# Kernel tuning notes

Hardware: AMD Instinct MI355X
Metric: run time of the kernel (lower is better)

The kernel has to match this reference:

```python
import jax, jax.numpy as jnp
import numpy as np

N = 16384          # replayed items
D_STATE = 2048     # state_dim
D_SEM = 1024       # semantic_dim
S = 4096           # num_semantic_slots
LR = 0.01
DIST_THRESH = 2.0


def setup_inputs() -> dict:
    key = jax.random.key(0)
    k1, k2, k3 = jax.random.split(key, 3)
    replayed_states = jax.random.normal(k1, (N, D_STATE), dtype=jnp.float32)
    replayed_rewards = jax.random.normal(k2, (N,), dtype=jnp.float32)
    # small weight scale so projected content std ~0.05 -> nearest distances
    # straddle the 2.0 threshold and both branches get exercised
    W = jax.random.normal(k3, (D_SEM, D_STATE), dtype=jnp.float32) * (0.05 / np.sqrt(D_STATE))
    b = jnp.zeros((D_SEM,), dtype=jnp.float32)
    semantic_traces = jnp.zeros((S, D_SEM), dtype=jnp.float32)
    trace_strengths = jnp.zeros((S,), dtype=jnp.float32)
    return {
        "replayed_states": replayed_states,
        "replayed_rewards": replayed_rewards,
        "W": W,
        "b": b,
        "semantic_traces": semantic_traces,
        "trace_strengths": trace_strengths,
    }


def _consolidate(content_all, rewards, traces0, strengths0):
    slot_ids = jnp.arange(S, dtype=jnp.int32)

    def step(carry, xs):
        traces, strengths, ptr, num = carry
        content, reward = xs
        reward = jnp.abs(reward)
        valid = jnp.minimum(num, S)
        # euclidean distances to valid slots (invalid -> +inf)
        d = jnp.sqrt(jnp.sum((traces - content[None, :]) ** 2, axis=1))
        d = jnp.where(slot_ids < valid, d, jnp.inf)
        nearest = jnp.argmin(d).astype(jnp.int32)
        nearest_dist = d[nearest]
        do_update = (num > 0) & (nearest_dist < DIST_THRESH)

        # branch A: EMA update of nearest slot
        eff_lr = LR * (1.0 + reward)
        delta = content - traces[nearest]
        traces_u = traces.at[nearest].add(delta * eff_lr)
        strengths_u = strengths.at[nearest].add(1.0)

        # branch B: insert at ring-buffer ptr
        traces_i = traces.at[ptr].set(content)
        strengths_i = strengths.at[ptr].set(1.0)
        ptr_i = (ptr + 1) % S
        num_i = jnp.minimum(num + 1, S)

        traces_n = jnp.where(do_update, traces_u, traces_i)
        strengths_n = jnp.where(do_update, strengths_u, strengths_i)
        ptr_n = jnp.where(do_update, ptr, ptr_i)
        num_n = jnp.where(do_update, num, num_i)
        return (traces_n, strengths_n, ptr_n, num_n), None

    init = (traces0, strengths0, jnp.int32(0), jnp.int32(0))
    (traces, strengths, ptr, num), _ = jax.lax.scan(step, init, (content_all, rewards))
    return traces, strengths, num


def reference(replayed_states, replayed_rewards, W, b, semantic_traces, trace_strengths):
    # projection: nn.Linear -> x @ W.T + b
    content_all = replayed_states @ W.T + b  # (N, D_SEM)
    traces, strengths, num = _consolidate(
        content_all, replayed_rewards, semantic_traces, trace_strengths
    )
    valid_mask = (jnp.arange(S) < jnp.minimum(num, S)).astype(jnp.float32)
    denom = jnp.maximum(valid_mask.sum(), 1.0)
    mean_strength = jnp.where(num > 0, (strengths * valid_mask).sum() / denom, 0.0)
    num_consolidated = jnp.int32(N)  # every item either updates or inserts
    return traces, strengths, num, num_consolidated, mean_strength


if __name__ == "__main__":
    out = reference(**setup_inputs())
    print([getattr(o, "shape", o) for o in out])
```

## Files before the change

### kernel.cpp

```cpp
#include <hip/hip_runtime.h>
#include <cstdint>
#include <cstddef>

#define N_ITEMS 16384
#define D_STATE 2048
#define D_SEM   1024
#define S_SLOTS 4096
#define DTHRESH 2.0f

#define B_ITEMS 256
#define NBLK    (N_ITEMS / B_ITEMS)
#define CHUNK_BLKS 16
#define CHUNK_ITEMS (B_ITEMS * CHUNK_BLKS)

typedef unsigned long long u64;
typedef unsigned int u32;

__global__ __launch_bounds__(256)
void gemm_kernel(const float* __restrict__ A, const float* __restrict__ W,
                 const float* __restrict__ bias, float* __restrict__ C) {
  __shared__ float As[16][68];
  __shared__ float Bs[16][68];
  const int t = threadIdx.x;
  const int ty = t >> 4, tx = t & 15;
  const int i0 = blockIdx.x * 64, j0 = blockIdx.y * 64;
  const int lrow = t >> 2, lcol = (t & 3) << 2;
  float acc[4][4] = {{0.f}};
  const float* ap = A + (size_t)(i0 + lrow) * D_STATE + lcol;
  const float* wp = W + (size_t)(j0 + lrow) * D_STATE + lcol;
  for (int k0 = 0; k0 < D_STATE; k0 += 16) {
    float4 av = *(const float4*)(ap + k0);
    float4 wv = *(const float4*)(wp + k0);
    __syncthreads();
    As[lcol + 0][lrow] = av.x; As[lcol + 1][lrow] = av.y;
    As[lcol + 2][lrow] = av.z; As[lcol + 3][lrow] = av.w;
    Bs[lcol + 0][lrow] = wv.x; Bs[lcol + 1][lrow] = wv.y;
    Bs[lcol + 2][lrow] = wv.z; Bs[lcol + 3][lrow] = wv.w;
    __syncthreads();
#pragma unroll
    for (int kk = 0; kk < 16; kk++) {
      float a[4], b[4];
#pragma unroll
      for (int y = 0; y < 4; y++) a[y] = As[kk][ty * 4 + y];
#pragma unroll
      for (int x = 0; x < 4; x++) b[x] = Bs[kk][tx * 4 + x];
#pragma unroll
      for (int y = 0; y < 4; y++)
#pragma unroll
        for (int x = 0; x < 4; x++) acc[y][x] = fmaf(a[y], b[x], acc[y][x]);
    }
  }
#pragma unroll
  for (int y = 0; y < 4; y++)
#pragma unroll
    for (int x = 0; x < 4; x++) {
      const int col = j0 + tx * 4 + x;
      C[(size_t)(i0 + ty * 4 + y) * D_SEM + col] = acc[y][x] + bias[col];
    }
}

__global__ __launch_bounds__(256)
void gram_kernel(const float* __restrict__ Cc, float* __restrict__ G) {
  const int z = blockIdx.z;
  const float* A = Cc + (size_t)z * B_ITEMS * D_SEM;
  __shared__ float As[16][68];
  __shared__ float Bs[16][68];
  const int t = threadIdx.x;
  const int ty = t >> 4, tx = t & 15;
  const int i0 = blockIdx.x * 64, j0 = blockIdx.y * 64;
  const int lrow = t >> 2, lcol = (t & 3) << 2;
  float acc[4][4] = {{0.f}};
  const float* ap = A + (size_t)(i0 + lrow) * D_SEM + lcol;
  const float* wp = A + (size_t)(j0 + lrow) * D_SEM + lcol;
  for (int k0 = 0; k0 < D_SEM; k0 += 16) {
    float4 av = *(const float4*)(ap + k0);
    float4 wv = *(const float4*)(wp + k0);
    __syncthreads();
    As[lcol + 0][lrow] = av.x; As[lcol + 1][lrow] = av.y;
    As[lcol + 2][lrow] = av.z; As[lcol + 3][lrow] = av.w;
    Bs[lcol + 0][lrow] = wv.x; Bs[lcol + 1][lrow] = wv.y;
    Bs[lcol + 2][lrow] = wv.z; Bs[lcol + 3][lrow] = wv.w;
    __syncthreads();
#pragma unroll
    for (int kk = 0; kk < 16; kk++) {
      float a[4], b[4];
#pragma unroll
      for (int y = 0; y < 4; y++) a[y] = As[kk][ty * 4 + y];
#pragma unroll
      for (int x = 0; x < 4; x++) b[x] = Bs[kk][tx * 4 + x];
#pragma unroll
      for (int y = 0; y < 4; y++)
#pragma unroll
        for (int x = 0; x < 4; x++) acc[y][x] = fmaf(a[y], b[x], acc[y][x]);
    }
  }
  float* Gz = G + (size_t)z * B_ITEMS * B_ITEMS;
#pragma unroll
  for (int y = 0; y < 4; y++)
#pragma unroll
    for (int x = 0; x < 4; x++)
      Gz[(size_t)(i0 + ty * 4 + y) * B_ITEMS + j0 + tx * 4 + x] = acc[y][x];
}

__global__ __launch_bounds__(256)
void pgemm_kernel(const float* __restrict__ A,
                  const float* __restrict__ T,
                  const float* __restrict__ n_g,
                  float* __restrict__ Q,
                  const int* __restrict__ state) {
  const int limit = min(state[0] + B_ITEMS, S_SLOTS);
  const int j0 = blockIdx.y * 64;
  if (j0 >= limit) return;
  __shared__ float As[16][68];
  __shared__ float Bs[16][68];
  const int t = threadIdx.x;
  const int ty = t >> 4, tx = t & 15;
  const int i0 = blockIdx.x * 64;
  const int lrow = t >> 2, lcol = (t & 3) << 2;
  float acc[4][4] = {{0.f}};
  const float* ap = A + (size_t)(i0 + lrow) * D_SEM + lcol;
  const float* wp = T + (size_t)(j0 + lrow) * D_SEM + lcol;
  for (int k0 = 0; k0 < D_SEM; k0 += 16) {
    float4 av = *(const float4*)(ap + k0);
    float4 wv = *(const float4*)(wp + k0);
    __syncthreads();
    As[lcol + 0][lrow] = av.x; As[lcol + 1][lrow] = av.y;
    As[lcol + 2][lrow] = av.z; As[lcol + 3][lrow] = av.w;
    Bs[lcol + 0][lrow] = wv.x; Bs[lcol + 1][lrow] = wv.y;
    Bs[lcol + 2][lrow] = wv.z; Bs[lcol + 3][lrow] = wv.w;
    __syncthreads();
#pragma unroll
    for (int kk = 0; kk < 16; kk++) {
      float a[4], b[4];
#pragma unroll
      for (int y = 0; y < 4; y++) a[y] = As[kk][ty * 4 + y];
#pragma unroll
      for (int x = 0; x < 4; x++) b[x] = Bs[kk][tx * 4 + x];
#pragma unroll
      for (int y = 0; y < 4; y++)
#pragma unroll
        for (int x = 0; x < 4; x++) acc[y][x] = fmaf(a[y], b[x], acc[y][x]);
    }
  }
#pragma unroll
  for (int y = 0; y < 4; y++)
#pragma unroll
    for (int x = 0; x < 4; x++) {
      const int col = j0 + tx * 4 + x;
      Q[(size_t)(i0 + ty * 4 + y) * S_SLOTS + col] = n_g[col] - 2.0f * acc[y][x];
    }
}

__global__ __launch_bounds__(256)
void init_kernel(const float* __restrict__ traces0, float* __restrict__ out,
                 float* __restrict__ n_g, int* __restrict__ state) {
  __shared__ float wsum[4];
  const int s = blockIdx.x, t = threadIdx.x;
  const int lane = t & 63, wave = t >> 6;
  float4 v = *(const float4*)(traces0 + (size_t)s * D_SEM + 4 * t);
  *(float4*)(out + (size_t)s * D_SEM + 4 * t) = v;
  float nn = v.x * v.x + v.y * v.y + v.z * v.z + v.w * v.w;
#pragma unroll
  for (int o = 32; o; o >>= 1) nn += __shfl_down(nn, o, 64);
  if (lane == 0) wsum[wave] = nn;
  __syncthreads();
  if (t == 0) n_g[s] = wsum[0] + wsum[1] + wsum[2] + wsum[3];
  if (s == 0 && t == 0) { state[0] = 0; state[1] = 0; }
}

__global__ __launch_bounds__(512)
void scan_kernel(float* __restrict__ Q, const float* __restrict__ Gb,
                 const float* __restrict__ rewards, const float* __restrict__ n_g,
                 int* __restrict__ state, u64* __restrict__ decs) {
  __shared__ float n_l[S_SLOTS];
  __shared__ float rew[B_ITEMS];
  __shared__ float gdiag[B_ITEMS];
  __shared__ u64 partials[8];
  __shared__ u32 pub_slotupd;
  __shared__ float pub_lr, pub_nold, pub_nnew;
  __shared__ int sh_num[2], sh_ptr[2];
  __shared__ u32 dslot[B_ITEMS];
  __shared__ float dlr[B_ITEMS];

  const int t = threadIdx.x;
  const int lane = t & 63, wave = t >> 6;

  for (int s = t; s < S_SLOTS; s += 512) n_l[s] = n_g[s];
  if (t < B_ITEMS) {
    rew[t] = rewards[t];
    gdiag[t] = Gb[(size_t)t * B_ITEMS + t];
  }
  if (t == 0) { sh_num[0] = state[0]; sh_ptr[0] = state[1]; }
  float4 n0 = *(const float4*)(Q + 8 * t);
  float4 n1 = *(const float4*)(Q + 8 * t + 4);
  __syncthreads();

  int par = 0;
  for (int i = 0; i < B_ITEMS; i++) {
    float4 c0 = n0, c1 = n1;
    if (i + 1 < B_ITEMS) {
      n0 = *(const float4*)(Q + (size_t)(i + 1) * S_SLOTS + 8 * t);
      n1 = *(const float4*)(Q + (size_t)(i + 1) * S_SLOTS + 8 * t + 4);
    }
    const int num = sh_num[par];
    const float gi = gdiag[i];
    const int s0 = 8 * t;
    u64 best = ~0ull;
#define KEYC(comp, idx) { const int ss = s0 + idx; \
    if (ss < num) { const float d2 = fmaxf(comp + gi, 0.f); \
      const u64 key = ((u64)__float_as_uint(d2) << 32) | (u32)ss; \
      if (key < best) best = key; } }
    KEYC(c0.x, 0) KEYC(c0.y, 1) KEYC(c0.z, 2) KEYC(c0.w, 3)
    KEYC(c1.x, 4) KEYC(c1.y, 5) KEYC(c1.z, 6) KEYC(c1.w, 7)
#undef KEYC
#pragma unroll
    for (int o = 32; o; o >>= 1) {
      const u64 v = __shfl_down(best, o, 64);
      if (v < best) best = v;
    }
    if (lane == 0) partials[wave] = best;
    __syncthreads();

    if (t == 0) {
      u64 bk = partials[0];
#pragma unroll
      for (int wv = 1; wv < 8; wv++) if (partials[wv] < bk) bk = partials[wv];
      const float d2b = __uint_as_float((u32)(bk >> 32));
      const int nslot = (int)(u32)bk;
      const int numc = sh_num[par], ptrc = sh_ptr[par];
      const bool upd = (numc > 0) && (sqrtf(d2b) < DTHRESH);
      const float lr = __fmul_rn(0.01f, __fadd_rn(1.0f, fabsf(rew[i])));
      const int slot = upd ? nslot : ptrc;
      const float n_old = n_l[slot];
      float n_new;
      if (upd) {
        const float omr = 1.0f - lr;
        const float pcur = 0.5f * (n_old + gi - d2b);
        n_new = omr * omr * n_old + 2.0f * lr * omr * pcur + lr * lr * gi;
        sh_num[par ^ 1] = numc; sh_ptr[par ^ 1] = ptrc;
      } else {
        n_new = gi;
        sh_num[par ^ 1] = min(numc + 1, S_SLOTS);
        sh_ptr[par ^ 1] = (ptrc + 1) & (S_SLOTS - 1);
      }
      n_l[slot] = n_new;
      dslot[i] = (u32)slot | (upd ? 0x80000000u : 0u);
      dlr[i] = lr;
      pub_slotupd = (u32)slot | (upd ? 0x80000000u : 0u);
      pub_lr = lr; pub_nold = n_old; pub_nnew = n_new;
    }
    __syncthreads();

    const u32 su = pub_slotupd;
    const int slot = (int)(su & 0x7FFFFFFFu);
    const bool upd = (su & 0x80000000u) != 0;
    const float lr = pub_lr, n_old = pub_nold, n_new = pub_nnew;
    const float omr = 1.0f - lr;
    if (i + 1 < B_ITEMS && t == (slot >> 3)) {
      const float gnext = Gb[(size_t)i * B_ITEMS + (i + 1)];
      const int k = slot & 7;
      float q_old = k == 0 ? n0.x : k == 1 ? n0.y : k == 2 ? n0.z : k == 3 ? n0.w
                  : k == 4 ? n1.x : k == 5 ? n1.y : k == 6 ? n1.z : n1.w;
      const float p_old = 0.5f * (n_old - q_old);
      const float p_new = upd ? (omr * p_old + lr * gnext) : gnext;
      const float q_new = n_new - 2.0f * p_new;
      switch (k) {
        case 0: n0.x = q_new; break; case 1: n0.y = q_new; break;
        case 2: n0.z = q_new; break; case 3: n0.w = q_new; break;
        case 4: n1.x = q_new; break; case 5: n1.y = q_new; break;
        case 6: n1.z = q_new; break; default: n1.w = q_new; break;
      }
    }
    if (t > i + 1 && t < B_ITEMS) {
      const float gv = Gb[(size_t)i * B_ITEMS + t];
      float* qp = Q + (size_t)t * S_SLOTS + slot;
      float p_new;
      if (upd) {
        const float p_old = 0.5f * (n_old - *qp);
        p_new = omr * p_old + lr * gv;
      } else {
        p_new = gv;
      }
      *qp = n_new - 2.0f * p_new;
    }
    par ^= 1;
    __syncthreads();
  }

  if (t == 0) { state[0] = sh_num[par]; state[1] = sh_ptr[par]; }
  if (t < B_ITEMS)
    decs[t] = ((u64)__float_as_uint(dlr[t]) << 32) | (u64)dslot[t];
}

__global__ __launch_bounds__(256)
void apply_kernel(const float* __restrict__ content,
                  const u64* __restrict__ decs,
                  float* __restrict__ traces,
                  float* __restrict__ n_g) {
  __shared__ u32 aslot[B_ITEMS];
  __shared__ float alr[B_ITEMS];
  __shared__ float betas[B_ITEMS];
  __shared__ int notowner;
  __shared__ float wsum[4];
  const int t = threadIdx.x, j = blockIdx.x;
  const int lane = t & 63, wave = t >> 6;
  const u64 d = decs[t];
  aslot[t] = (u32)(d & 0xFFFFFFFFull);
  alr[t] = __uint_as_float((u32)(d >> 32));
  if (t == 0) notowner = 0;
  __syncthreads();
  const u32 myslot = aslot[j] & 0x7FFFFFFFu;
  if (t > j && (aslot[t] & 0x7FFFFFFFu) == myslot) notowner = 1;
  __syncthreads();
  if (notowner) return;

  float alpha = 1.f, beta = 0.f;
  for (int k = 0; k < B_ITEMS; k++) {
    const u32 a = aslot[k];
    if ((a & 0x7FFFFFFFu) == myslot) {
      const float lr = alr[k];
      if (a & 0x80000000u) {
        const float om = 1.f - lr;
        alpha *= om; beta *= om;
        if (t == k) beta += lr;
      } else {
        alpha = 0.f; beta = (t == k) ? 1.f : 0.f;
      }
    }
  }
  betas[t] = beta;
  __syncthreads();

  float4 v = *(const float4*)(traces + (size_t)myslot * D_SEM + 4 * t);
  v.x *= alpha; v.y *= alpha; v.z *= alpha; v.w *= alpha;
  for (int k = 0; k < B_ITEMS; k++) {
    if ((aslot[k] & 0x7FFFFFFFu) == myslot) {
      const float bk = betas[k];
      const float4 c = *(const float4*)(content + (size_t)k * D_SEM + 4 * t);
      v.x = fmaf(bk, c.x, v.x); v.y = fmaf(bk, c.y, v.y);
      v.z = fmaf(bk, c.z, v.z); v.w = fmaf(bk, c.w, v.w);
    }
  }
  *(float4*)(traces + (size_t)myslot * D_SEM + 4 * t) = v;
  float nn = v.x * v.x + v.y * v.y + v.z * v.z + v.w * v.w;
#pragma unroll
  for (int o = 32; o; o >>= 1) nn += __shfl_down(nn, o, 64);
  if (lane == 0) wsum[wave] = nn;
  __syncthreads();
  if (t == 0) n_g[myslot] = wsum[0] + wsum[1] + wsum[2] + wsum[3];
}

__global__ __launch_bounds__(256)
void finalize_kernel(const float* __restrict__ strengths0,
                     const u64* __restrict__ decs,
                     const int* __restrict__ state, float* __restrict__ out) {
  __shared__ float str[S_SLOTS];
  __shared__ u32 dbuf[2048];
  __shared__ float wsum[4];
  const int t = threadIdx.x, lane = t & 63, wave = t >> 6;
  for (int s = t; s < S_SLOTS; s += 256) str[s] = strengths0[s];
  __syncthreads();
  for (int c = 0; c < N_ITEMS; c += 2048) {
    for (int k = t; k < 2048; k += 256) dbuf[k] = (u32)(decs[c + k] & 0xFFFFFFFFull);
    __syncthreads();
    if (t == 0) {
      for (int k = 0; k < 2048; k++) {
        const u32 dd = dbuf[k];
        const int slot = (int)(dd & 0x7FFFFFFFu);
        if (dd & 0x80000000u) str[slot] += 1.f; else str[slot] = 1.f;
      }
    }
    __syncthreads();
  }
  const int num = state[0];
  float* outs = out + (size_t)S_SLOTS * D_SEM;
  float lsum = 0.f;
  for (int s = t; s < S_SLOTS; s += 256) {
    const float v = str[s];
    outs[s] = v;
    if (s < num) lsum += v;
  }
#pragma unroll
  for (int o = 32; o; o >>= 1) lsum += __shfl_down(lsum, o, 64);
  if (lane == 0) wsum[wave] = lsum;
  __syncthreads();
  if (t == 0) {
    const float total = wsum[0] + wsum[1] + wsum[2] + wsum[3];
    float denom = (float)num;
    if (denom < 1.f) denom = 1.f;
    outs[S_SLOTS + 0] = (float)num;
    outs[S_SLOTS + 1] = (float)N_ITEMS;
    outs[S_SLOTS + 2] = (num > 0) ? (total / denom) : 0.f;
  }
}

extern "C" void kernel_launch(void* const* d_in, const int* in_sizes, int n_in,
                              void* d_out, int out_size, void* d_ws, size_t ws_size,
                              hipStream_t stream) {
  const float* states  = (const float*)d_in[0];
  const float* rewards = (const float*)d_in[1];
  const float* W       = (const float*)d_in[2];
  const float* bias    = (const float*)d_in[3];
  const float* traces0 = (const float*)d_in[4];
  const float* str0    = (const float*)d_in[5];
  float* out = (float*)d_out;

  char* p = (char*)d_ws;
  float* cbuf = (float*)p;                 p += (size_t)CHUNK_ITEMS * D_SEM * 4;
  float* Q    = (float*)p;                 p += (size_t)B_ITEMS * S_SLOTS * 4;
  float* Gb   = (float*)p;                 p += (size_t)CHUNK_BLKS * B_ITEMS * B_ITEMS * 4;
  float* n_g  = (float*)p;                 p += (size_t)S_SLOTS * 4;
  u64*   decs = (u64*)p;                   p += (size_t)N_ITEMS * 8;
  int*   state = (int*)p;

  init_kernel<<<S_SLOTS, 256, 0, stream>>>(traces0, out, n_g, state);

  for (int c = 0; c < N_ITEMS / CHUNK_ITEMS; c++) {
    gemm_kernel<<<dim3(CHUNK_ITEMS / 64, D_SEM / 64), 256, 0, stream>>>(
        states + (size_t)c * CHUNK_ITEMS * D_STATE, W, bias, cbuf);
    gram_kernel<<<dim3(4, 4, CHUNK_BLKS), 256, 0, stream>>>(cbuf, Gb);
    for (int bb = 0; bb < CHUNK_BLKS; bb++) {
      const int b = c * CHUNK_BLKS + bb;
      const float* cblk = cbuf + (size_t)bb * B_ITEMS * D_SEM;
      const float* Gblk = Gb + (size_t)bb * B_ITEMS * B_ITEMS;
      pgemm_kernel<<<dim3(4, S_SLOTS / 64), 256, 0, stream>>>(cblk, out, n_g, Q, state);
      scan_kernel<<<1, 512, 0, stream>>>(Q, Gblk, rewards + (size_t)b * B_ITEMS,
                                         n_g, state, decs + (size_t)b * B_ITEMS);
      apply_kernel<<<B_ITEMS, 256, 0, stream>>>(cblk, decs + (size_t)b * B_ITEMS,
                                                out, n_g);
    }
  }
  finalize_kernel<<<1, 256, 0, stream>>>(str0, decs, state, out);
}
```

Baseline: 36.82 ms.

## Restructure serial scan to register-resident norms with one barrier per item

The per-item scan now keeps slot norms and dot products in registers (16 slots per thread, 256 threads) and stores raw dot products P instead of precomputed distances Q. Every thread redundantly computes the argmin decision, so the single-thread decision step and one of the two barriers per item go away. pgemm zero-fills the inactive tiles, and finalize replaces the serial strength replay with parallel atomics (last insert index plus count of later updates). The trade-off is more registers per thread and redundant scalar work on every thread.

```diff
diff --git a/kernel.cpp b/kernel.cpp
--- a/kernel.cpp
+++ b/kernel.cpp
@@ -105,17 +105,23 @@
 __global__ __launch_bounds__(256)
 void pgemm_kernel(const float* __restrict__ A,
                   const float* __restrict__ T,
-                  const float* __restrict__ n_g,
-                  float* __restrict__ Q,
+                  float* __restrict__ P,
                   const int* __restrict__ state) {
   const int limit = min(state[0] + B_ITEMS, S_SLOTS);
   const int j0 = blockIdx.y * 64;
-  if (j0 >= limit) return;
+  const int i0 = blockIdx.x * 64;
+  const int t = threadIdx.x;
+  const int ty = t >> 4, tx = t & 15;
+  if (j0 >= limit) {
+    const float4 z = {0.f, 0.f, 0.f, 0.f};
+    const int col = j0 + tx * 4;
+#pragma unroll
+    for (int y = 0; y < 4; y++)
+      *(float4*)(P + (size_t)(i0 + ty * 4 + y) * S_SLOTS + col) = z;
+    return;
+  }
   __shared__ float As[16][68];
   __shared__ float Bs[16][68];
-  const int t = threadIdx.x;
-  const int ty = t >> 4, tx = t & 15;
-  const int i0 = blockIdx.x * 64;
   const int lrow = t >> 2, lcol = (t & 3) << 2;
   float acc[4][4] = {{0.f}};
   const float* ap = A + (size_t)(i0 + lrow) * D_SEM + lcol;
@@ -145,10 +151,8 @@
 #pragma unroll
   for (int y = 0; y < 4; y++)
 #pragma unroll
-    for (int x = 0; x < 4; x++) {
-      const int col = j0 + tx * 4 + x;
-      Q[(size_t)(i0 + ty * 4 + y) * S_SLOTS + col] = n_g[col] - 2.0f * acc[y][x];
-    }
+    for (int x = 0; x < 4; x++)
+      P[(size_t)(i0 + ty * 4 + y) * S_SLOTS + j0 + tx * 4 + x] = acc[y][x];
 }
 
 __global__ __launch_bounds__(256)
@@ -168,128 +172,119 @@
   if (s == 0 && t == 0) { state[0] = 0; state[1] = 0; }
 }
 
-__global__ __launch_bounds__(512)
-void scan_kernel(float* __restrict__ Q, const float* __restrict__ Gb,
+__global__ __launch_bounds__(256)
+void scan_kernel(float* __restrict__ P, const float* __restrict__ Gb,
                  const float* __restrict__ rewards, const float* __restrict__ n_g,
                  int* __restrict__ state, u64* __restrict__ decs) {
-  __shared__ float n_l[S_SLOTS];
-  __shared__ float rew[B_ITEMS];
-  __shared__ float gdiag[B_ITEMS];
-  __shared__ u64 partials[8];
-  __shared__ u32 pub_slotupd;
-  __shared__ float pub_lr, pub_nold, pub_nnew;
-  __shared__ int sh_num[2], sh_ptr[2];
-  __shared__ u32 dslot[B_ITEMS];
-  __shared__ float dlr[B_ITEMS];
-
+  __shared__ u64 partials[2][4];
   const int t = threadIdx.x;
   const int lane = t & 63, wave = t >> 6;
-
-  for (int s = t; s < S_SLOTS; s += 512) n_l[s] = n_g[s];
-  if (t < B_ITEMS) {
-    rew[t] = rewards[t];
-    gdiag[t] = Gb[(size_t)t * B_ITEMS + t];
-  }
-  if (t == 0) { sh_num[0] = state[0]; sh_ptr[0] = state[1]; }
-  float4 n0 = *(const float4*)(Q + 8 * t);
-  float4 n1 = *(const float4*)(Q + 8 * t + 4);
-  __syncthreads();
-
-  int par = 0;
+  const int s_base = t << 4;
+
+  int num = state[0];
+  int ptr = state[1];
+
+  float n_reg[16];
+#pragma unroll
+  for (int k = 0; k < 16; k += 4) {
+    float4 nv = *(const float4*)(n_g + s_base + k);
+    n_reg[k + 0] = (s_base + k + 0 < num) ? nv.x : __uint_as_float(0x7F800000u);
+    n_reg[k + 1] = (s_base + k + 1 < num) ? nv.y : __uint_as_float(0x7F800000u);
+    n_reg[k + 2] = (s_base + k + 2 < num) ? nv.z : __uint_as_float(0x7F800000u);
+    n_reg[k + 3] = (s_base + k + 3 < num) ? nv.w : __uint_as_float(0x7F800000u);
+  }
+
+  float p_cur[16], p_nxt[16];
+#pragma unroll
+  for (int k = 0; k < 16; k += 4) {
+    float4 v = *(const float4*)(P + s_base + k);
+    p_cur[k] = v.x; p_cur[k + 1] = v.y; p_cur[k + 2] = v.z; p_cur[k + 3] = v.w;
+  }
+#pragma unroll
+  for (int k = 0; k < 16; k++) p_nxt[k] = 0.f;
+
+  float greg = Gb[t];
+  float gi   = Gb[0];
+  float ri   = rewards[0];
+
+  u32 my_slot = 0; float my_lr = 0.f;
+
   for (int i = 0; i < B_ITEMS; i++) {
-    float4 c0 = n0, c1 = n1;
+    float gi_n = 0.f, ri_n = 0.f, gnext = 0.f, greg_n = 0.f;
     if (i + 1 < B_ITEMS) {
-      n0 = *(const float4*)(Q + (size_t)(i + 1) * S_SLOTS + 8 * t);
-      n1 = *(const float4*)(Q + (size_t)(i + 1) * S_SLOTS + 8 * t + 4);
-    }
-    const int num = sh_num[par];
-    const float gi = gdiag[i];
-    const int s0 = 8 * t;
+      gi_n   = Gb[(size_t)(i + 1) * B_ITEMS + (i + 1)];
+      ri_n   = rewards[i + 1];
+      gnext  = Gb[(size_t)i * B_ITEMS + (i + 1)];
+      greg_n = Gb[(size_t)(i + 1) * B_ITEMS + t];
+#pragma unroll
+      for (int k = 0; k < 16; k += 4) {
+        float4 v = *(const float4*)(P + (size_t)(i + 1) * S_SLOTS + s_base + k);
+        p_nxt[k] = v.x; p_nxt[k + 1] = v.y; p_nxt[k + 2] = v.z; p_nxt[k + 3] = v.w;
+      }
+    }
+
     u64 best = ~0ull;
-#define KEYC(comp, idx) { const int ss = s0 + idx; \
-    if (ss < num) { const float d2 = fmaxf(comp + gi, 0.f); \
-      const u64 key = ((u64)__float_as_uint(d2) << 32) | (u32)ss; \
-      if (key < best) best = key; } }
-    KEYC(c0.x, 0) KEYC(c0.y, 1) KEYC(c0.z, 2) KEYC(c0.w, 3)
-    KEYC(c1.x, 4) KEYC(c1.y, 5) KEYC(c1.z, 6) KEYC(c1.w, 7)
-#undef KEYC
+#pragma unroll
+    for (int k = 0; k < 16; k++) {
+      const float d2 = fmaxf(fmaf(-2.0f, p_cur[k], n_reg[k] + gi), 0.f);
+      const u64 key = ((u64)__float_as_uint(d2) << 32) | (u32)(s_base + k);
+      if (key < best) best = key;
+    }
 #pragma unroll
     for (int o = 32; o; o >>= 1) {
       const u64 v = __shfl_down(best, o, 64);
       if (v < best) best = v;
     }
-    if (lane == 0) partials[wave] = best;
-    __syncthreads();
-
-    if (t == 0) {
-      u64 bk = partials[0];
-#pragma unroll
-      for (int wv = 1; wv < 8; wv++) if (partials[wv] < bk) bk = partials[wv];
-      const float d2b = __uint_as_float((u32)(bk >> 32));
-      const int nslot = (int)(u32)bk;
-      const int numc = sh_num[par], ptrc = sh_ptr[par];
-      const bool upd = (numc > 0) && (sqrtf(d2b) < DTHRESH);
-      const float lr = __fmul_rn(0.01f, __fadd_rn(1.0f, fabsf(rew[i])));
-      const int slot = upd ? nslot : ptrc;
-      const float n_old = n_l[slot];
-      float n_new;
-      if (upd) {
-        const float omr = 1.0f - lr;
-        const float pcur = 0.5f * (n_old + gi - d2b);
-        n_new = omr * omr * n_old + 2.0f * lr * omr * pcur + lr * lr * gi;
-        sh_num[par ^ 1] = numc; sh_ptr[par ^ 1] = ptrc;
-      } else {
-        n_new = gi;
-        sh_num[par ^ 1] = min(numc + 1, S_SLOTS);
-        sh_ptr[par ^ 1] = (ptrc + 1) & (S_SLOTS - 1);
+    if (lane == 0) partials[i & 1][wave] = best;
+    __syncthreads();
+
+    u64 bk = partials[i & 1][0];
+    { u64 v = partials[i & 1][1]; if (v < bk) bk = v;
+      v = partials[i & 1][2]; if (v < bk) bk = v;
+      v = partials[i & 1][3]; if (v < bk) bk = v; }
+    const float d2b = __uint_as_float((u32)(bk >> 32));
+    const int nslot = (int)(u32)bk;
+    const bool upd = (num > 0) && (sqrtf(d2b) < DTHRESH);
+    const float lr = __fmul_rn(0.01f, __fadd_rn(1.0f, fabsf(ri)));
+    const int slot = upd ? nslot : ptr;
+    const float omr = 1.0f - lr;
+    if (!upd) { num = min(num + 1, S_SLOTS); ptr = (ptr + 1) & (S_SLOTS - 1); }
+    if (i == t) { my_slot = (u32)slot | (upd ? 0x80000000u : 0u); my_lr = lr; }
+
+    if ((slot >> 4) == t) {
+#define OWNFIX(K) { const float nold = n_reg[K]; float pn = p_nxt[K]; float nnew; \
+      if (upd) { const float pc = 0.5f * (nold + gi - d2b); \
+        nnew = omr * omr * nold + 2.0f * lr * omr * pc + lr * lr * gi; \
+        pn = fmaf(omr, pn, lr * gnext); } \
+      else { nnew = gi; pn = gnext; } \
+      n_reg[K] = nnew; p_nxt[K] = pn; }
+      switch (slot & 15) {
+        case 0:  OWNFIX(0)  break; case 1:  OWNFIX(1)  break;
+        case 2:  OWNFIX(2)  break; case 3:  OWNFIX(3)  break;
+        case 4:  OWNFIX(4)  break; case 5:  OWNFIX(5)  break;
+        case 6:  OWNFIX(6)  break; case 7:  OWNFIX(7)  break;
+        case 8:  OWNFIX(8)  break; case 9:  OWNFIX(9)  break;
+        case 10: OWNFIX(10) break; case 11: OWNFIX(11) break;
+        case 12: OWNFIX(12) break; case 13: OWNFIX(13) break;
+        case 14: OWNFIX(14) break; default: OWNFIX(15) break;
       }
-      n_l[slot] = n_new;
-      dslot[i] = (u32)slot | (upd ? 0x80000000u : 0u);
-      dlr[i] = lr;
-      pub_slotupd = (u32)slot | (upd ? 0x80000000u : 0u);
-      pub_lr = lr; pub_nold = n_old; pub_nnew = n_new;
-    }
-    __syncthreads();
-
-    const u32 su = pub_slotupd;
-    const int slot = (int)(su & 0x7FFFFFFFu);
-    const bool upd = (su & 0x80000000u) != 0;
-    const float lr = pub_lr, n_old = pub_nold, n_new = pub_nnew;
-    const float omr = 1.0f - lr;
-    if (i + 1 < B_ITEMS && t == (slot >> 3)) {
-      const float gnext = Gb[(size_t)i * B_ITEMS + (i + 1)];
-      const int k = slot & 7;
-      float q_old = k == 0 ? n0.x : k == 1 ? n0.y : k == 2 ? n0.z : k == 3 ? n0.w
-                  : k == 4 ? n1.x : k == 5 ? n1.y : k == 6 ? n1.z : n1.w;
-      const float p_old = 0.5f * (n_old - q_old);
-      const float p_new = upd ? (omr * p_old + lr * gnext) : gnext;
-      const float q_new = n_new - 2.0f * p_new;
-      switch (k) {
-        case 0: n0.x = q_new; break; case 1: n0.y = q_new; break;
-        case 2: n0.z = q_new; break; case 3: n0.w = q_new; break;
-        case 4: n1.x = q_new; break; case 5: n1.y = q_new; break;
-        case 6: n1.z = q_new; break; default: n1.w = q_new; break;
-      }
-    }
-    if (t > i + 1 && t < B_ITEMS) {
-      const float gv = Gb[(size_t)i * B_ITEMS + t];
-      float* qp = Q + (size_t)t * S_SLOTS + slot;
-      float p_new;
-      if (upd) {
-        const float p_old = 0.5f * (n_old - *qp);
-        p_new = omr * p_old + lr * gv;
-      } else {
-        p_new = gv;
-      }
-      *qp = n_new - 2.0f * p_new;
-    }
-    par ^= 1;
-    __syncthreads();
-  }
-
-  if (t == 0) { state[0] = sh_num[par]; state[1] = sh_ptr[par]; }
-  if (t < B_ITEMS)
-    decs[t] = ((u64)__float_as_uint(dlr[t]) << 32) | (u64)dslot[t];
+#undef OWNFIX
+    }
+
+    if (t >= i + 2) {
+      float* qp = P + (size_t)t * S_SLOTS + slot;
+      if (upd) *qp = fmaf(omr, *qp, __fmul_rn(lr, greg));
+      else     *qp = greg;
+    }
+
+#pragma unroll
+    for (int k = 0; k < 16; k++) p_cur[k] = p_nxt[k];
+    gi = gi_n; ri = ri_n; greg = greg_n;
+    __syncthreads();
+  }
+
+  if (t == 0) { state[0] = num; state[1] = ptr; }
+  decs[t] = ((u64)__float_as_uint(my_lr) << 32) | (u64)my_slot;
 }
 
 __global__ __launch_bounds__(256)
@@ -354,29 +349,29 @@
 void finalize_kernel(const float* __restrict__ strengths0,
                      const u64* __restrict__ decs,
                      const int* __restrict__ state, float* __restrict__ out) {
-  __shared__ float str[S_SLOTS];
-  __shared__ u32 dbuf[2048];
+  __shared__ int last_ins[S_SLOTS];
+  __shared__ int cnt[S_SLOTS];
   __shared__ float wsum[4];
   const int t = threadIdx.x, lane = t & 63, wave = t >> 6;
-  for (int s = t; s < S_SLOTS; s += 256) str[s] = strengths0[s];
-  __syncthreads();
-  for (int c = 0; c < N_ITEMS; c += 2048) {
-    for (int k = t; k < 2048; k += 256) dbuf[k] = (u32)(decs[c + k] & 0xFFFFFFFFull);
-    __syncthreads();
-    if (t == 0) {
-      for (int k = 0; k < 2048; k++) {
-        const u32 dd = dbuf[k];
-        const int slot = (int)(dd & 0x7FFFFFFFu);
-        if (dd & 0x80000000u) str[slot] += 1.f; else str[slot] = 1.f;
-      }
-    }
-    __syncthreads();
-  }
+  for (int s = t; s < S_SLOTS; s += 256) { last_ins[s] = -1; cnt[s] = 0; }
+  __syncthreads();
+  for (int k = t; k < N_ITEMS; k += 256) {
+    const u32 dd = (u32)(decs[k] & 0xFFFFFFFFull);
+    if (!(dd & 0x80000000u)) atomicMax(&last_ins[(int)dd], k);
+  }
+  __syncthreads();
+  for (int k = t; k < N_ITEMS; k += 256) {
+    const u32 dd = (u32)(decs[k] & 0xFFFFFFFFull);
+    const int slot = (int)(dd & 0x7FFFFFFFu);
+    if ((dd & 0x80000000u) && k > last_ins[slot]) atomicAdd(&cnt[slot], 1);
+  }
+  __syncthreads();
   const int num = state[0];
   float* outs = out + (size_t)S_SLOTS * D_SEM;
   float lsum = 0.f;
   for (int s = t; s < S_SLOTS; s += 256) {
-    const float v = str[s];
+    const float base = (last_ins[s] >= 0) ? 1.f : strengths0[s];
+    const float v = base + (float)cnt[s];
     outs[s] = v;
     if (s < num) lsum += v;
   }
@@ -407,7 +402,7 @@
 
   char* p = (char*)d_ws;
   float* cbuf = (float*)p;                 p += (size_t)CHUNK_ITEMS * D_SEM * 4;
-  float* Q    = (float*)p;                 p += (size_t)B_ITEMS * S_SLOTS * 4;
+  float* P    = (float*)p;                 p += (size_t)B_ITEMS * S_SLOTS * 4;
   float* Gb   = (float*)p;                 p += (size_t)CHUNK_BLKS * B_ITEMS * B_ITEMS * 4;
   float* n_g  = (float*)p;                 p += (size_t)S_SLOTS * 4;
   u64*   decs = (u64*)p;                   p += (size_t)N_ITEMS * 8;
@@ -423,8 +418,8 @@
       const int b = c * CHUNK_BLKS + bb;
       const float* cblk = cbuf + (size_t)bb * B_ITEMS * D_SEM;
       const float* Gblk = Gb + (size_t)bb * B_ITEMS * B_ITEMS;
-      pgemm_kernel<<<dim3(4, S_SLOTS / 64), 256, 0, stream>>>(cblk, out, n_g, Q, state);
-      scan_kernel<<<1, 512, 0, stream>>>(Q, Gblk, rewards + (size_t)b * B_ITEMS,
+      pgemm_kernel<<<dim3(4, S_SLOTS / 64), 256, 0, stream>>>(cblk, out, P, state);
+      scan_kernel<<<1, 256, 0, stream>>>(P, Gblk, rewards + (size_t)b * B_ITEMS,
                                          n_g, state, decs + (size_t)b * B_ITEMS);
       apply_kernel<<<B_ITEMS, 256, 0, stream>>>(cblk, decs + (size_t)b * B_ITEMS,
                                                 out, n_g);
```

Measured after the change: 34.58 ms. 1.06x faster.
